# Kernel tuning notes

Hardware: AMD Instinct MI355X
Metric: run time of the kernel (lower is better)

The kernel has to match this reference:

```python
import jax, jax.numpy as jnp
import numpy as np

B, M, E, NPOS, F, NHEAD, NLAYERS, DFF = 32, 512, 512, 1024, 768, 8, 2, 2048
S = M + 1

def _pe(embed, pad):
    pos = np.arange(pad, dtype=np.float32)[:, None]
    i = np.arange(embed)[None, :]
    ang = pos / np.power(10000.0, (i // 2 * 2.0) / embed)
    pe = np.where(i % 2 == 0, np.sin(ang), np.cos(ang))
    return jnp.asarray(pe, jnp.float32)

PE = _pe(E, M)  # [M, E] sinusoidal table, matches pos_embedding()

def _ln(x, w, b, eps=1e-5):
    mu = x.mean(-1, keepdims=True)
    var = ((x - mu) ** 2).mean(-1, keepdims=True)
    return (x - mu) / jnp.sqrt(var + eps) * w + b

def _mha(x, wi, bi, wo, bo):
    # x: [L, N, E] where L is the attended axis (torch seq dim)
    L, N, Em = x.shape
    Dh = Em // NHEAD
    q, k, v = jnp.split(x @ wi.T + bi, 3, axis=-1)
    q = q.reshape(L, N, NHEAD, Dh) * np.float32(1.0 / np.sqrt(Dh))
    k = k.reshape(L, N, NHEAD, Dh)
    v = v.reshape(L, N, NHEAD, Dh)
    att = jax.nn.softmax(jnp.einsum('lnhd,mnhd->nhlm', q, k), axis=-1)
    o = jnp.einsum('nhlm,mnhd->lnhd', att, v).reshape(L, N, Em)
    return o @ wo.T + bo

def _encoder(x, enc):
    wi, bi, wo, bo, ln1w, ln1b, ln2w, ln2b, w1, b1, w2, b2 = enc
    for l in range(NLAYERS):  # post-norm TransformerEncoderLayer, ReLU, eval mode
        x = _ln(x + _mha(x, wi[l], bi[l], wo[l], bo[l]), ln1w[l], ln1b[l])
        h = jax.nn.relu(x @ w1[l].T + b1[l]) @ w2[l].T + b2[l]
        x = _ln(x + h, ln2w[l], ln2b[l])
    return x

def _forward(pos1, pos2, bert_feature, final_base, emb_table, enc, w_model, w_disc, b_disc):
    emb_table = emb_table.at[0].set(0.0)  # padding_idx=0
    embed = emb_table[pos2] + PE          # [B, M, E]
    starts, ends = pos1[..., 0], pos1[..., 1]
    # loop breaks at first span with end==0: valid = prefix of nonzero ends
    valid = jnp.cumprod((ends != 0).astype(jnp.int32), axis=1).astype(bool)
    k = jnp.arange(M)
    cover = valid[:, :, None] & (starts[:, :, None] <= k) & (k < ends[:, :, None])  # [B, Mspan, Mpos]
    # later spans overwrite earlier ones -> take max covering span index
    span_id = jnp.max(jnp.where(cover, jnp.arange(M)[None, :, None], -1), axis=1)  # [B, Mpos]
    filled = jnp.take_along_axis(embed, jnp.clip(span_id, 0, M - 1)[..., None], axis=1)
    final = jnp.where(span_id[..., None] >= 0, filled, final_base)  # [B, M, E]
    cls = jnp.broadcast_to(emb_table[1], (B, 1, E))
    x = jnp.concatenate([cls, final], axis=1)  # [B, S, E]; torch encoder treats dim0 as seq
    x = _encoder(x, enc)
    pos_feature = jnp.tanh(x @ w_model.T)      # [B, S, F]
    z = jnp.concatenate([bert_feature, pos_feature], axis=-1) @ w_disc.T + b_disc
    return jax.nn.sigmoid(z)                   # [B, S, 1]

def setup_inputs():
    key = jax.random.key(0)
    ks = jax.random.split(key, 12)
    sc = 0.02
    n_valid, chunk = 120, 4  # contiguous spans [4j, 4j+4) for j < 120, then end==0 terminator
    j = np.arange(M)
    starts = np.where(j < n_valid, j * chunk, 0)
    ends = np.where(j < n_valid, j * chunk + chunk, 0)
    pos1 = np.broadcast_to(np.stack([starts, ends], -1), (B, M, 2)).astype(np.int32)
    return {
        'pos1': jnp.asarray(pos1),
        'pos2': jax.random.randint(ks[0], (B, M), 2, NPOS),
        'bert_feature': jax.random.normal(ks[1], (B, S, F), jnp.float32),
        'final_base': jax.random.uniform(ks[2], (B, M, E), jnp.float32),
        'emb_table': jax.random.normal(ks[3], (NPOS, E), jnp.float32) * sc,
        'enc_in_proj_w': jax.random.normal(ks[4], (NLAYERS, 3 * E, E), jnp.float32) * sc,
        'enc_in_proj_b': jnp.zeros((NLAYERS, 3 * E), jnp.float32),
        'enc_out_proj_w': jax.random.normal(ks[5], (NLAYERS, E, E), jnp.float32) * sc,
        'enc_out_proj_b': jnp.zeros((NLAYERS, E), jnp.float32),
        'enc_ln1_w': jnp.ones((NLAYERS, E), jnp.float32),
        'enc_ln1_b': jnp.zeros((NLAYERS, E), jnp.float32),
        'enc_ln2_w': jnp.ones((NLAYERS, E), jnp.float32),
        'enc_ln2_b': jnp.zeros((NLAYERS, E), jnp.float32),
        'enc_ffn_w1': jax.random.normal(ks[6], (NLAYERS, DFF, E), jnp.float32) * sc,
        'enc_ffn_b1': jnp.zeros((NLAYERS, DFF), jnp.float32),
        'enc_ffn_w2': jax.random.normal(ks[7], (NLAYERS, E, DFF), jnp.float32) * sc,
        'enc_ffn_b2': jnp.zeros((NLAYERS, E), jnp.float32),
        'w_model': jax.random.normal(ks[8], (F, E), jnp.float32) * sc,
        'w_disc': jax.random.normal(ks[9], (1, 2 * F), jnp.float32) * sc,
        'b_disc': jnp.zeros((1,), jnp.float32),
    }

def reference(pos1, pos2, bert_feature, final_base, emb_table,
              enc_in_proj_w, enc_in_proj_b, enc_out_proj_w, enc_out_proj_b,
              enc_ln1_w, enc_ln1_b, enc_ln2_w, enc_ln2_b,
              enc_ffn_w1, enc_ffn_b1, enc_ffn_w2, enc_ffn_b2,
              w_model, w_disc, b_disc):
    enc = (enc_in_proj_w, enc_in_proj_b, enc_out_proj_w, enc_out_proj_b,
           enc_ln1_w, enc_ln1_b, enc_ln2_w, enc_ln2_b,
           enc_ffn_w1, enc_ffn_b1, enc_ffn_w2, enc_ffn_b2)
    return _forward(pos1, pos2, bert_feature, final_base, emb_table, enc, w_model, w_disc, b_disc)
```

## Files before the change

kernel.cpp:

```cpp
#include <hip/hip_runtime.h>
#include <hip/hip_bf16.h>

#define B_   32
#define M_   512
#define E_   512
#define S_   513
#define T_   (B_ * S_)
#define TP_  16512
#define NH_  8
#define DH_  64
#define F_   768
#define DFF_ 2048

#define GMT_ 129

typedef short short8 __attribute__((ext_vector_type(8)));
typedef float floatx4 __attribute__((ext_vector_type(4)));

__device__ __forceinline__ float bf2f(unsigned short u) {
    return __uint_as_float(((unsigned int)u) << 16);
}
__device__ __forceinline__ unsigned short f2b_rne(float f) {
    unsigned int u = __float_as_uint(f);
    unsigned int r = u + 0x7FFF + ((u >> 16) & 1);
    return (unsigned short)(r >> 16);
}
__device__ __forceinline__ void gload16(const void* g, void* l) {
    __builtin_amdgcn_global_load_lds(
        (const __attribute__((address_space(1))) void*)g,
        (__attribute__((address_space(3))) void*)l, 16, 0, 0);
}
__device__ __forceinline__ void wait_vm0() { __builtin_amdgcn_s_waitcnt(0x0F70); }
__device__ __forceinline__ void wait_vm4() { __builtin_amdgcn_s_waitcnt(0x0F74); }

__global__ void span_kernel(const int* __restrict__ pos1, int* __restrict__ span) {
    int b = blockIdx.x;
    __shared__ int st[M_], en[M_];
    __shared__ int nv;
    int tid = threadIdx.x;
    for (int j = tid; j < M_; j += 256) {
        st[j] = pos1[(b * M_ + j) * 2];
        en[j] = pos1[(b * M_ + j) * 2 + 1];
    }
    __syncthreads();
    if (tid == 0) {
        int n = M_;
        for (int j = 0; j < M_; ++j) if (en[j] == 0) { n = j; break; }
        nv = n;
    }
    __syncthreads();
    int n = nv;
    for (int k = tid; k < M_; k += 256) {
        int best = -1;
        for (int j = 0; j < n; ++j)
            if (st[j] <= k && k < en[j]) best = j;
        span[b * M_ + k] = best;
    }
}

__global__ void f2b5_kernel(const float* __restrict__ s0, const float* __restrict__ s1,
                            const float* __restrict__ s2, const float* __restrict__ s3,
                            const float* __restrict__ s4,
                            unsigned short* __restrict__ dst,
                            int c0, int c1, int c2, int c3, int c4) {
    int i = (blockIdx.x * 256 + threadIdx.x) * 4;
    if (i >= c4) return;
    const float* src; int off;
    if      (i < c0) { src = s0; off = i; }
    else if (i < c1) { src = s1; off = i - c0; }
    else if (i < c2) { src = s2; off = i - c1; }
    else if (i < c3) { src = s3; off = i - c2; }
    else             { src = s4; off = i - c3; }
    float4 v = *(const float4*)(src + off);
    ushort4 o;
    o.x = f2b_rne(v.x); o.y = f2b_rne(v.y);
    o.z = f2b_rne(v.z); o.w = f2b_rne(v.w);
    *(ushort4*)(dst + i) = o;
}

__global__ void build_x(const float* __restrict__ emb,
                        const int* __restrict__ pos2,
                        const float* __restrict__ fbase,
                        const int* __restrict__ span,
                        float* __restrict__ x,
                        unsigned short* __restrict__ xb) {
    long long idx = (long long)blockIdx.x * blockDim.x + threadIdx.x;
    if (idx >= (long long)T_ * E_) return;
    int e = (int)(idx % E_);
    int t = (int)(idx / E_);
    int s = t % S_;
    int b = t / S_;
    float val;
    if (s == 0) {
        val = emb[E_ + e];
    } else {
        int k = s - 1;
        int sid = span[b * M_ + k];
        if (sid >= 0) {
            int p = pos2[b * M_ + sid];
            float ex = (float)((e >> 1) << 1) * (1.0f / 512.0f);
            float ang = (float)sid * exp2f(-ex * 13.287712379549449f);
            float pe = (e & 1) ? cosf(ang) : sinf(ang);
            val = emb[(size_t)p * E_ + e] + pe;
        } else {
            val = fbase[((size_t)b * M_ + k) * E_ + e];
        }
    }
    x[idx] = val;
    xb[idx] = f2b_rne(val);
}

template <int ACT, int KT>
__global__ __launch_bounds__(256, 3) void gemm_bf16(const unsigned short* __restrict__ A,
                                                    const unsigned short* __restrict__ W,
                                                    const float* __restrict__ bias,
                                                    unsigned short* __restrict__ Cb,
                                                    int T, int O) {
    constexpr int K = KT;
    constexpr int NSTEP = K / 32;
    __shared__ __align__(16) unsigned short sA[3][128 * 32];
    __shared__ __align__(16) unsigned short sB[3][128 * 32];
    int tid = threadIdx.x;
    int lane = tid & 63, wv = tid >> 6;
    int wr = (wv >> 1) * 64, wc = (wv & 1) * 64;

    int gn = O / 128;
    int per_panel = 8 * gn;
    int id = blockIdx.x;
    int p = id / per_panel;
    int r = id - p * per_panel;
    int mrem = GMT_ - p * 8; if (mrem > 8) mrem = 8;
    int mt = p * 8 + r % mrem;
    int nt = r / mrem;
    int t0 = mt * 128, o0 = nt * 128;

    floatx4 acc[4][4] = {};

    const unsigned short* Ag = A + (size_t)(t0 + wv * 32 + (lane >> 2)) * K + (lane & 3) * 8;
    const unsigned short* Bg = W + (size_t)(o0 + wv * 32 + (lane >> 2)) * K + (lane & 3) * 8;
    const size_t row16 = (size_t)16 * K;
    int fr = lane & 15;
    int fk = (lane >> 4) * 8;

    {
        unsigned short* dA = &sA[0][wv * 1024];
        unsigned short* dB = &sB[0][wv * 1024];
        gload16(Ag, dA);
        gload16(Ag + row16, dA + 512);
        gload16(Bg, dB);
        gload16(Bg + row16, dB + 512);
    }
    {
        unsigned short* dA = &sA[1][wv * 1024];
        unsigned short* dB = &sB[1][wv * 1024];
        gload16(Ag + 32, dA);
        gload16(Ag + row16 + 32, dA + 512);
        gload16(Bg + 32, dB);
        gload16(Bg + row16 + 32, dB + 512);
    }

    int cur = 0, nx2 = 2;
    for (int s = 0; s < NSTEP; ++s) {
        if (s < NSTEP - 1) wait_vm4();
        else               wait_vm0();
        __syncthreads();

        if (s + 2 < NSTEP) {
            const int k = (s + 2) * 32;
            unsigned short* dA = &sA[nx2][wv * 1024];
            unsigned short* dB = &sB[nx2][wv * 1024];
            gload16(Ag + k, dA);
            gload16(Ag + row16 + k, dA + 512);
            gload16(Bg + k, dB);
            gload16(Bg + row16 + k, dB + 512);
        }

        short8 af[4], bfr[4];
#pragma unroll
        for (int i = 0; i < 4; ++i)
            af[i] = *(const short8*)&sA[cur][(wr + i * 16 + fr) * 32 + fk];
#pragma unroll
        for (int j = 0; j < 4; ++j)
            bfr[j] = *(const short8*)&sB[cur][(wc + j * 16 + fr) * 32 + fk];
#pragma unroll
        for (int i = 0; i < 4; ++i)
#pragma unroll
            for (int j = 0; j < 4; ++j)
                acc[i][j] = __builtin_amdgcn_mfma_f32_16x16x32_bf16(af[i], bfr[j], acc[i][j], 0, 0, 0);

        cur = (cur == 2) ? 0 : cur + 1;
        nx2 = (nx2 == 2) ? 0 : nx2 + 1;
    }

    int cr = (lane >> 4) * 4;
    int cc = lane & 15;
#pragma unroll
    for (int i = 0; i < 4; ++i) {
#pragma unroll
        for (int j = 0; j < 4; ++j) {
            int gn_ = o0 + wc + j * 16 + cc;
            float bv = bias ? bias[gn_] : 0.f;
#pragma unroll
            for (int rr = 0; rr < 4; ++rr) {
                int gm_ = t0 + wr + i * 16 + cr + rr;
                if (gm_ >= T) continue;
                float v = acc[i][j][rr] + bv;
                if (ACT == 1) v = fmaxf(v, 0.f);
                if (ACT == 2) v = tanhf(v);
                Cb[(size_t)gm_ * O + gn_] = f2b_rne(v);
            }
        }
    }
}

__global__ __launch_bounds__(64) void attn_mfma(const unsigned short* __restrict__ qkv,
                                                unsigned short* __restrict__ o) {
    __shared__ __align__(16) unsigned short vt[64 * 40];
    __shared__ __align__(16) unsigned short ps[32 * 40];
    int s = blockIdx.x, h = blockIdx.y;
    int lane = threadIdx.x;
    int hd = h * 64;
    int fr = lane & 15, fq = lane >> 4;

    {
        int m = lane >> 1;
        int d0 = (lane & 1) * 32;
        const unsigned short* vrow = qkv + ((size_t)m * S_ + s) * 1536 + 1024 + hd + d0;
        short8 v0 = *(const short8*)(vrow);
        short8 v1 = *(const short8*)(vrow + 8);
        short8 v2 = *(const short8*)(vrow + 16);
        short8 v3 = *(const short8*)(vrow + 24);
#pragma unroll
        for (int j = 0; j < 8; ++j) {
            vt[(d0 + j) * 40 + m]      = (unsigned short)v0[j];
            vt[(d0 + 8 + j) * 40 + m]  = (unsigned short)v1[j];
            vt[(d0 + 16 + j) * 40 + m] = (unsigned short)v2[j];
            vt[(d0 + 24 + j) * 40 + m] = (unsigned short)v3[j];
        }
    }

    floatx4 c[2][2] = {};
#pragma unroll
    for (int ks = 0; ks < 2; ++ks) {
        short8 aq[2], bk[2];
#pragma unroll
        for (int lt = 0; lt < 2; ++lt) {
            int l = lt * 16 + fr;
            aq[lt] = *(const short8*)(qkv + ((size_t)l * S_ + s) * 1536 + hd + ks * 32 + fq * 8);
        }
#pragma unroll
        for (int mt = 0; mt < 2; ++mt) {
            int m = mt * 16 + fr;
            bk[mt] = *(const short8*)(qkv + ((size_t)m * S_ + s) * 1536 + 512 + hd + ks * 32 + fq * 8);
        }
#pragma unroll
        for (int lt = 0; lt < 2; ++lt)
#pragma unroll
            for (int mt = 0; mt < 2; ++mt)
                c[lt][mt] = __builtin_amdgcn_mfma_f32_16x16x32_bf16(aq[lt], bk[mt], c[lt][mt], 0, 0, 0);
    }

#pragma unroll
    for (int lt = 0; lt < 2; ++lt) {
#pragma unroll
        for (int r = 0; r < 4; ++r) {
            float a = c[lt][0][r] * 0.125f;
            float b = c[lt][1][r] * 0.125f;
            float mx = fmaxf(a, b);
#pragma unroll
            for (int off = 1; off < 16; off <<= 1) mx = fmaxf(mx, __shfl_xor(mx, off));
            float ea = expf(a - mx), eb = expf(b - mx);
            float sm = ea + eb;
#pragma unroll
            for (int off = 1; off < 16; off <<= 1) sm += __shfl_xor(sm, off);
            float inv = 1.f / sm;
            int l = lt * 16 + fq * 4 + r;
            ps[l * 40 + fr]      = f2b_rne(ea * inv);
            ps[l * 40 + 16 + fr] = f2b_rne(eb * inv);
        }
    }
    __syncthreads();

    short8 pa[2], vb[4];
#pragma unroll
    for (int lt = 0; lt < 2; ++lt)
        pa[lt] = *(const short8*)&ps[(lt * 16 + fr) * 40 + fq * 8];
#pragma unroll
    for (int dt = 0; dt < 4; ++dt)
        vb[dt] = *(const short8*)&vt[(dt * 16 + fr) * 40 + fq * 8];

    floatx4 oa[2][4] = {};
#pragma unroll
    for (int lt = 0; lt < 2; ++lt)
#pragma unroll
        for (int dt = 0; dt < 4; ++dt)
            oa[lt][dt] = __builtin_amdgcn_mfma_f32_16x16x32_bf16(pa[lt], vb[dt], oa[lt][dt], 0, 0, 0);

#pragma unroll
    for (int lt = 0; lt < 2; ++lt)
#pragma unroll
        for (int dt = 0; dt < 4; ++dt)
#pragma unroll
            for (int r = 0; r < 4; ++r) {
                int l = lt * 16 + fq * 4 + r;
                o[((size_t)l * S_ + s) * E_ + hd + dt * 16 + fr] = f2b_rne(oa[lt][dt][r]);
            }
}

__global__ __launch_bounds__(256) void add_ln(float* __restrict__ x,
                                              unsigned short* __restrict__ xb,
                                              const unsigned short* __restrict__ h,
                                              const float* __restrict__ w,
                                              const float* __restrict__ b) {
    int t = blockIdx.x;
    float* xr = x + (size_t)t * E_;
    const unsigned short* hr = h + (size_t)t * E_;
    int i0 = threadIdx.x * 2;
    float2 xv = *(const float2*)&xr[i0];
    ushort2 hv = *(const ushort2*)&hr[i0];
    float v0 = xv.x + bf2f(hv.x), v1 = xv.y + bf2f(hv.y);

    __shared__ float red[4];
    float sum = v0 + v1;
    for (int off = 32; off; off >>= 1) sum += __shfl_down(sum, off);
    if ((threadIdx.x & 63) == 0) red[threadIdx.x >> 6] = sum;
    __syncthreads();
    float mu = (red[0] + red[1] + red[2] + red[3]) * (1.0f / E_);
    __syncthreads();

    float d0 = v0 - mu, d1 = v1 - mu;
    float qs = d0 * d0 + d1 * d1;
    for (int off = 32; off; off >>= 1) qs += __shfl_down(qs, off);
    if ((threadIdx.x & 63) == 0) red[threadIdx.x >> 6] = qs;
    __syncthreads();
    float var = (red[0] + red[1] + red[2] + red[3]) * (1.0f / E_);
    float rstd = rsqrtf(var + 1e-5f);

    float o0 = d0 * rstd * w[i0]     + b[i0];
    float o1 = d1 * rstd * w[i0 + 1] + b[i0 + 1];
    *(float2*)&xr[i0] = make_float2(o0, o1);
    xb[(size_t)t * E_ + i0]     = f2b_rne(o0);
    xb[(size_t)t * E_ + i0 + 1] = f2b_rne(o1);
}

__global__ __launch_bounds__(256) void disc_kernel(const float* __restrict__ bert,
                                                   const unsigned short* __restrict__ pf,
                                                   const float* __restrict__ wd,
                                                   const float* __restrict__ bd,
                                                   float* __restrict__ out) {
    int t = blockIdx.x;
    float s = 0.f;
    for (int f = threadIdx.x; f < F_; f += 256) {
        s += bert[(size_t)t * F_ + f] * wd[f];
        s += bf2f(pf[(size_t)t * F_ + f]) * wd[F_ + f];
    }
    for (int off = 32; off; off >>= 1) s += __shfl_down(s, off);
    __shared__ float red[4];
    if ((threadIdx.x & 63) == 0) red[threadIdx.x >> 6] = s;
    __syncthreads();
    if (threadIdx.x == 0) {
        float z = red[0] + red[1] + red[2] + red[3] + bd[0];
        out[t] = 1.f / (1.f + expf(-z));
    }
}

extern "C" void kernel_launch(void* const* d_in, const int* in_sizes, int n_in,
                              void* d_out, int out_size, void* d_ws, size_t ws_size,
                              hipStream_t stream) {
    const int*   pos1 = (const int*)d_in[0];
    const int*   pos2 = (const int*)d_in[1];
    const float* bert = (const float*)d_in[2];
    const float* fb   = (const float*)d_in[3];
    const float* emb  = (const float*)d_in[4];
    const float* wi   = (const float*)d_in[5];
    const float* bi   = (const float*)d_in[6];
    const float* wo   = (const float*)d_in[7];
    const float* bo   = (const float*)d_in[8];
    const float* ln1w = (const float*)d_in[9];
    const float* ln1b = (const float*)d_in[10];
    const float* ln2w = (const float*)d_in[11];
    const float* ln2b = (const float*)d_in[12];
    const float* w1   = (const float*)d_in[13];
    const float* b1   = (const float*)d_in[14];
    const float* w2   = (const float*)d_in[15];
    const float* b2   = (const float*)d_in[16];
    const float* wm   = (const float*)d_in[17];
    const float* wd   = (const float*)d_in[18];
    const float* bd   = (const float*)d_in[19];
    float* out = (float*)d_out;

    float* ws   = (float*)d_ws;
    int*   span = (int*)ws;
    float* x    = ws + 16384;
    unsigned short* xb  = (unsigned short*)(x + (size_t)T_ * 512);
    unsigned short* atb = xb + (size_t)TP_ * 512;
    unsigned short* hb  = atb + (size_t)TP_ * 512;
    unsigned short* U   = hb + (size_t)T_ * 512;
    unsigned short* qkvb = U;
    unsigned short* h1b  = U;
    unsigned short* pfb  = U;
    unsigned short* wib  = U + (size_t)TP_ * 2048;
    const int NWI = 2 * 1536 * 512;
    const int NWO = 2 * 512 * 512;
    const int NW1 = 2 * 2048 * 512;
    const int NW2 = 2 * 512 * 2048;
    const int NWM = 768 * 512;
    unsigned short* wob = wib + NWI;
    unsigned short* w1b = wob + NWO;
    unsigned short* w2b = w1b + NW1;
    unsigned short* wmb = w2b + NW2;

    span_kernel<<<B_, 256, 0, stream>>>(pos1, span);
    {
        int c0 = NWI, c1 = c0 + NWO, c2 = c1 + NW1, c3 = c2 + NW2, c4 = c3 + NWM;
        f2b5_kernel<<<(c4 / 4 + 255) / 256, 256, 0, stream>>>(wi, wo, w1, w2, wm, wib,
                                                              c0, c1, c2, c3, c4);
    }
    build_x<<<(int)(((long long)T_ * 512 + 255) / 256), 256, 0, stream>>>(emb, pos2, fb, span, x, xb);

    for (int l = 0; l < 2; ++l) {
        gemm_bf16<0, 512><<<GMT_ * (1536 / 128), 256, 0, stream>>>(
            xb, wib + (size_t)l * 1536 * 512, bi + l * 1536, qkvb, T_, 1536);
        attn_mfma<<<dim3(S_, NH_), 64, 0, stream>>>(qkvb, atb);
        gemm_bf16<0, 512><<<GMT_ * (512 / 128), 256, 0, stream>>>(
            atb, wob + (size_t)l * 512 * 512, bo + l * 512, hb, T_, 512);
        add_ln<<<T_, 256, 0, stream>>>(x, xb, hb, ln1w + l * 512, ln1b + l * 512);
        gemm_bf16<1, 512><<<GMT_ * (2048 / 128), 256, 0, stream>>>(
            xb, w1b + (size_t)l * 2048 * 512, b1 + l * 2048, h1b, T_, 2048);
        gemm_bf16<0, 2048><<<GMT_ * (512 / 128), 256, 0, stream>>>(
            h1b, w2b + (size_t)l * 512 * 2048, b2 + l * 512, hb, T_, 512);
        add_ln<<<T_, 256, 0, stream>>>(x, xb, hb, ln2w + l * 512, ln2b + l * 512);
    }
    gemm_bf16<2, 512><<<GMT_ * (768 / 128), 256, 0, stream>>>(
        xb, wmb, nullptr, pfb, T_, 768);
    disc_kernel<<<T_, 256, 0, stream>>>(bert, pfb, wd, bd, out);
}
```

Baseline: 805.7 us.

## Load GEMM operand fragments directly from global memory into registers, dropping LDS staging

Replaces the triple-buffered LDS pipeline (async global-to-LDS loads plus barriers) in the bf16 GEMM with per-wave direct global loads of MFMA fragments into registers, prefetching one k-step ahead. This removes the shared-memory footprint and the per-step __syncthreads. In exchange each wave now fetches its own A and B fragments from global/L2 with no sharing across the block's waves, which doubles global traffic per block and uses narrow 16-byte strided row accesses.

```diff
diff --git a/kernel.cpp b/kernel.cpp
--- a/kernel.cpp
+++ b/kernel.cpp
@@ -25,13 +25,6 @@
     unsigned int r = u + 0x7FFF + ((u >> 16) & 1);
     return (unsigned short)(r >> 16);
 }
-__device__ __forceinline__ void gload16(const void* g, void* l) {
-    __builtin_amdgcn_global_load_lds(
-        (const __attribute__((address_space(1))) void*)g,
-        (__attribute__((address_space(3))) void*)l, 16, 0, 0);
-}
-__device__ __forceinline__ void wait_vm0() { __builtin_amdgcn_s_waitcnt(0x0F70); }
-__device__ __forceinline__ void wait_vm4() { __builtin_amdgcn_s_waitcnt(0x0F74); }
 
 __global__ void span_kernel(const int* __restrict__ pos1, int* __restrict__ span) {
     int b = blockIdx.x;
@@ -117,9 +110,6 @@
                                                     unsigned short* __restrict__ Cb,
                                                     int T, int O) {
     constexpr int K = KT;
-    constexpr int NSTEP = K / 32;
-    __shared__ __align__(16) unsigned short sA[3][128 * 32];
-    __shared__ __align__(16) unsigned short sB[3][128 * 32];
     int tid = threadIdx.x;
     int lane = tid & 63, wv = tid >> 6;
     int wr = (wv >> 1) * 64, wc = (wv & 1) * 64;
@@ -134,62 +124,37 @@
     int nt = r / mrem;
     int t0 = mt * 128, o0 = nt * 128;
 
-    floatx4 acc[4][4] = {};
-
-    const unsigned short* Ag = A + (size_t)(t0 + wv * 32 + (lane >> 2)) * K + (lane & 3) * 8;
-    const unsigned short* Bg = W + (size_t)(o0 + wv * 32 + (lane >> 2)) * K + (lane & 3) * 8;
-    const size_t row16 = (size_t)16 * K;
     int fr = lane & 15;
     int fk = (lane >> 4) * 8;
 
-    {
-        unsigned short* dA = &sA[0][wv * 1024];
-        unsigned short* dB = &sB[0][wv * 1024];
-        gload16(Ag, dA);
-        gload16(Ag + row16, dA + 512);
-        gload16(Bg, dB);
-        gload16(Bg + row16, dB + 512);
-    }
-    {
-        unsigned short* dA = &sA[1][wv * 1024];
-        unsigned short* dB = &sB[1][wv * 1024];
-        gload16(Ag + 32, dA);
-        gload16(Ag + row16 + 32, dA + 512);
-        gload16(Bg + 32, dB);
-        gload16(Bg + row16 + 32, dB + 512);
-    }
-
-    int cur = 0, nx2 = 2;
-    for (int s = 0; s < NSTEP; ++s) {
-        if (s < NSTEP - 1) wait_vm4();
-        else               wait_vm0();
-        __syncthreads();
-
-        if (s + 2 < NSTEP) {
-            const int k = (s + 2) * 32;
-            unsigned short* dA = &sA[nx2][wv * 1024];
-            unsigned short* dB = &sB[nx2][wv * 1024];
-            gload16(Ag + k, dA);
-            gload16(Ag + row16 + k, dA + 512);
-            gload16(Bg + k, dB);
-            gload16(Bg + row16 + k, dB + 512);
-        }
-
-        short8 af[4], bfr[4];
+    const unsigned short* ap = A + (size_t)(t0 + wr + fr) * K + fk;
+    const unsigned short* bp = W + (size_t)(o0 + wc + fr) * K + fk;
+    const size_t r16 = (size_t)16 * K;
+
+    floatx4 acc[4][4] = {};
+
+    short8 ac[4], bc[4];
+#pragma unroll
+    for (int i = 0; i < 4; ++i) ac[i] = *(const short8*)(ap + i * r16);
+#pragma unroll
+    for (int j = 0; j < 4; ++j) bc[j] = *(const short8*)(bp + j * r16);
+
+#pragma unroll 2
+    for (int k0 = 0; k0 < K; k0 += 32) {
+        short8 an[4], bn[4];
+        if (k0 + 32 < K) {
+#pragma unroll
+            for (int i = 0; i < 4; ++i) an[i] = *(const short8*)(ap + i * r16 + k0 + 32);
+#pragma unroll
+            for (int j = 0; j < 4; ++j) bn[j] = *(const short8*)(bp + j * r16 + k0 + 32);
+        }
 #pragma unroll
         for (int i = 0; i < 4; ++i)
-            af[i] = *(const short8*)&sA[cur][(wr + i * 16 + fr) * 32 + fk];
-#pragma unroll
-        for (int j = 0; j < 4; ++j)
-            bfr[j] = *(const short8*)&sB[cur][(wc + j * 16 + fr) * 32 + fk];
-#pragma unroll
-        for (int i = 0; i < 4; ++i)
 #pragma unroll
             for (int j = 0; j < 4; ++j)
-                acc[i][j] = __builtin_amdgcn_mfma_f32_16x16x32_bf16(af[i], bfr[j], acc[i][j], 0, 0, 0);
-
-        cur = (cur == 2) ? 0 : cur + 1;
-        nx2 = (nx2 == 2) ? 0 : nx2 + 1;
+                acc[i][j] = __builtin_amdgcn_mfma_f32_16x16x32_bf16(ac[i], bc[j], acc[i][j], 0, 0, 0);
+#pragma unroll
+        for (int i = 0; i < 4; ++i) { ac[i] = an[i]; bc[i] = bn[i]; }
     }
 
     int cr = (lane >> 4) * 4;
```

Result: slower. 1.395 ms (+73.2%).
